# Kernel tuning notes

Measured on AMD Instinct MI355X. Metric: run time of the kernel, lower is better.

## Reference

```python
import jax, jax.numpy as jnp
import numpy as np

RANK = 16
ALPHA = 32.0
SCALING = ALPHA / RANK  # 2.0


def setup_inputs() -> dict:
    key = jax.random.key(0)
    k1, k2, k3, k4, k5 = jax.random.split(key, 5)
    B, S, D_IN, D_OUT = 4, 4096, 4096, 4096
    x = jax.random.normal(k1, (B, S, D_IN), dtype=jnp.float32)
    W = jax.random.normal(k2, (D_OUT, D_IN), dtype=jnp.float32) * 0.02
    b = jax.random.normal(k3, (D_OUT,), dtype=jnp.float32) * 0.02
    lora_A = jax.random.normal(k4, (RANK, D_IN), dtype=jnp.float32) * 0.02
    lora_B = jax.random.normal(k5, (D_OUT, RANK), dtype=jnp.float32) * 0.02
    return {"x": x, "W": W, "b": b, "lora_A": lora_A, "lora_B": lora_B}


def reference(x, W, b, lora_A, lora_B):
    # Base linear: y = x @ W^T + b
    base = jnp.einsum("bsd,od->bso", x, W) + b
    # LoRA delta: mathematically x @ (B @ A)^T * scaling == ((x @ A^T) @ B^T) * scaling.
    # We chain the two small rank-limited GEMMs (same math, efficient form).
    xa = jnp.einsum("bsd,rd->bsr", x, lora_A)           # [B,S,rank]
    lora_out = jnp.einsum("bsr,or->bso", xa, lora_B)    # [B,S,out]
    return base + SCALING * lora_out
```

## Files before the change

kernel.cpp:

```cpp
#include <hip/hip_runtime.h>
#include <hip/hip_bf16.h>
#include <cstdint>

constexpr int  KDIM  = 4096;
constexpr int  NDIM  = 4096;
constexpr long MDIM  = 16384;
constexpr int  RANK_ = 16;
constexpr float SCALE_ = 2.0f;

constexpr int BK = 64;
constexpr int NT = KDIM / BK;

using bf16x8 = __attribute__((ext_vector_type(8))) short;
using f32x4  = __attribute__((ext_vector_type(4))) float;

__device__ __forceinline__ void gload_lds16(const void* g, void* l) {
  __builtin_amdgcn_global_load_lds(
      (const __attribute__((address_space(1))) void*)g,
      (__attribute__((address_space(3))) void*)l, 16, 0, 0);
}

__device__ __forceinline__ unsigned short f2bf(float f) {
  union { float f; unsigned u; } v; v.f = f;
  unsigned r = v.u + 0x7FFFu + ((v.u >> 16) & 1u);
  return (unsigned short)(r >> 16);
}

#define LDF(P, OFF) (*reinterpret_cast<const bf16x8*>((P) + (OFF)))

__global__ __launch_bounds__(256) void fused_prep_kernel(
    const float* __restrict__ x,  const float* __restrict__ W,
    const float* __restrict__ lA, const float* __restrict__ lB,
    unsigned short* __restrict__ xb, unsigned short* __restrict__ Wp) {
  if (blockIdx.x < 512) {
    const long totW = (long)NDIM * KDIM / 8;
    for (long t = blockIdx.x * 256L + threadIdx.x; t < totW; t += 512L * 256) {
      const int o  = (int)(t / (KDIM / 8));
      const int d8 = (int)(t % (KDIM / 8)) * 8;
      const float4* w4 = reinterpret_cast<const float4*>(W + (size_t)o * KDIM + d8);
      float4 w0 = w4[0], w1 = w4[1];
      float acc[8] = {w0.x, w0.y, w0.z, w0.w, w1.x, w1.y, w1.z, w1.w};
#pragma unroll
      for (int r = 0; r < RANK_; ++r) {
        const float br = SCALE_ * lB[o * RANK_ + r];
        const float4* a4 = reinterpret_cast<const float4*>(lA + (size_t)r * KDIM + d8);
        float4 a0 = a4[0], a1 = a4[1];
        acc[0] += br * a0.x; acc[1] += br * a0.y; acc[2] += br * a0.z; acc[3] += br * a0.w;
        acc[4] += br * a1.x; acc[5] += br * a1.y; acc[6] += br * a1.z; acc[7] += br * a1.w;
      }
      uint4 o4;
      o4.x = (unsigned)f2bf(acc[0]) | ((unsigned)f2bf(acc[1]) << 16);
      o4.y = (unsigned)f2bf(acc[2]) | ((unsigned)f2bf(acc[3]) << 16);
      o4.z = (unsigned)f2bf(acc[4]) | ((unsigned)f2bf(acc[5]) << 16);
      o4.w = (unsigned)f2bf(acc[6]) | ((unsigned)f2bf(acc[7]) << 16);
      *reinterpret_cast<uint4*>(Wp + t * 8) = o4;
    }
  } else {
    const long totX = MDIM * KDIM / 8;
    for (long t = (blockIdx.x - 512) * 256L + threadIdx.x; t < totX;
         t += 3584L * 256) {
      const float4* p = reinterpret_cast<const float4*>(x + t * 8);
      float4 a = p[0], b = p[1];
      uint4 o4;
      o4.x = (unsigned)f2bf(a.x) | ((unsigned)f2bf(a.y) << 16);
      o4.y = (unsigned)f2bf(a.z) | ((unsigned)f2bf(a.w) << 16);
      o4.z = (unsigned)f2bf(b.x) | ((unsigned)f2bf(b.y) << 16);
      o4.w = (unsigned)f2bf(b.z) | ((unsigned)f2bf(b.w) << 16);
      *reinterpret_cast<uint4*>(xb + t * 8) = o4;
    }
  }
}

__global__ __launch_bounds__(512, 2) void gemm256_kernel(
    const unsigned short* __restrict__ A,
    const unsigned short* __restrict__ Bm,
    const float* __restrict__ bias,
    float* __restrict__ C) {
  __shared__ __align__(16) unsigned char lds[131072];

  const int tid  = threadIdx.x;
  const int wave = tid >> 6, lane = tid & 63;
  const int wm = wave >> 2, wn = wave & 3;
  const int r16 = lane & 15, hi = lane >> 4;
  const int swz5 = ((r16 >> 3) & 1) << 5;
  const int lrB = (wn & 1) * 64;

  const int orig = blockIdx.x;
  const int bid  = (orig & 7) * 128 + (orig >> 3);
  const int bcol = (bid & 15) * 256;
  const int brow = (bid >> 4) * 256;

  const int st_row = wave * 16 + (lane >> 2);
  const int st_col = ((lane & 3) * 8) ^ (((lane >> 5) & 1) << 4);
  const unsigned short* Asrc = A  + (size_t)(brow + st_row) * KDIM + st_col;
  const unsigned short* Bsrc = Bm + (size_t)(bcol + st_row) * KDIM + st_col;

  auto stageHalf = [&](unsigned char* base, int s, int tau) {
    const unsigned short* g = (s >= 2 ? Asrc + (size_t)(s - 2) * 128 * KDIM
                                      : Bsrc + (size_t)s * 128 * KDIM) + tau * BK;
    unsigned char* d = base + (wave << 10) + s * 16384;
    gload_lds16(g,      d);
    gload_lds16(g + 32, d + 8192);
  };

  const int laneoff = r16 * 64 + ((hi * 16) ^ swz5);
  const unsigned char* pA0 = lds + (2 + wm) * 16384 + laneoff;
  const unsigned char* pB0 = lds + (wn >> 1) * 16384 + lrB * 64 + laneoff;
  const unsigned char* pA1 = pA0 + 65536;
  const unsigned char* pB1 = pB0 + 65536;

  f32x4 acc[8][4];
#pragma unroll
  for (int m = 0; m < 8; ++m)
#pragma unroll
    for (int n = 0; n < 4; ++n) acc[m][n] = (f32x4){0.f, 0.f, 0.f, 0.f};

  unsigned char* const buf0 = lds;
  unsigned char* const buf1 = lds + 65536;

  stageHalf(buf0, 0, 0); stageHalf(buf0, 1, 0);
  stageHalf(buf0, 2, 0); stageHalf(buf0, 3, 0);
  stageHalf(buf1, 0, 1); stageHalf(buf1, 1, 1);
  asm volatile("s_waitcnt vmcnt(4)" ::: "memory");
  __builtin_amdgcn_s_barrier();

  bf16x8 xlo[4][2], xhi[4][2], wlo[2][2], whi[2][2];
#pragma unroll
  for (int m = 0; m < 4; ++m) {
    xlo[m][0] = LDF(pA0, m * 1024);
    xlo[m][1] = LDF(pA0, m * 1024 + 8192);
  }

#define KTILE(CB, NB, PA, PB, PAN, t)                                          \
  {                                                                            \
         \
    _Pragma("unroll")                                                          \
    for (int n = 0; n < 2; ++n) {                                              \
      wlo[n][0] = LDF(PB, n * 1024);                                           \
      wlo[n][1] = LDF(PB, n * 1024 + 8192);                                    \
    }                                                                          \
    _Pragma("unroll")                                                          \
    for (int n = 0; n < 2; ++n) {                                              \
      whi[n][0] = LDF(PB, (n + 2) * 1024);                                     \
      whi[n][1] = LDF(PB, (n + 2) * 1024 + 8192);                              \
    }                                                                          \
    if ((t) + 1 < NT) { stageHalf((NB), 2, (t) + 1);                           \
                        stageHalf((NB), 3, (t) + 1); }                         \
    __builtin_amdgcn_s_setprio(1);                                             \
    _Pragma("unroll")                                                          \
    for (int kk = 0; kk < 2; ++kk)                                             \
      _Pragma("unroll")                                                        \
      for (int m = 0; m < 4; ++m)                                              \
        _Pragma("unroll")                                                      \
        for (int n = 0; n < 2; ++n)                                            \
          acc[m][n] = __builtin_amdgcn_mfma_f32_16x16x32_bf16(                 \
              wlo[n][kk], xlo[m][kk], acc[m][n], 0, 0, 0);                     \
    __builtin_amdgcn_s_setprio(0);                                             \
    __builtin_amdgcn_s_barrier();                                              \
                               \
    _Pragma("unroll")                                                          \
    for (int m = 0; m < 4; ++m) {                                              \
      xhi[m][0] = LDF(PA, (m + 4) * 1024);                                     \
      xhi[m][1] = LDF(PA, (m + 4) * 1024 + 8192);                              \
    }                                                                          \
    __builtin_amdgcn_s_setprio(1);                                             \
    _Pragma("unroll")                                                          \
    for (int kk = 0; kk < 2; ++kk)                                             \
      _Pragma("unroll")                                                        \
      for (int m = 0; m < 4; ++m)                                              \
        _Pragma("unroll")                                                      \
        for (int n = 0; n < 2; ++n)                                            \
          acc[m][n + 2] = __builtin_amdgcn_mfma_f32_16x16x32_bf16(             \
              whi[n][kk], xlo[m][kk], acc[m][n + 2], 0, 0, 0);                 \
    __builtin_amdgcn_s_setprio(0);                                             \
    __builtin_amdgcn_s_barrier();                                              \
            \
    if ((t) + 2 < NT) { stageHalf((CB), 0, (t) + 2);                           \
                        stageHalf((CB), 1, (t) + 2); }                         \
    __builtin_amdgcn_s_setprio(1);                                             \
    _Pragma("unroll")                                                          \
    for (int kk = 0; kk < 2; ++kk)                                             \
      _Pragma("unroll")                                                        \
      for (int m = 0; m < 4; ++m)                                              \
        _Pragma("unroll")                                                      \
        for (int n = 0; n < 2; ++n)                                            \
          acc[m + 4][n + 2] = __builtin_amdgcn_mfma_f32_16x16x32_bf16(         \
              whi[n][kk], xhi[m][kk], acc[m + 4][n + 2], 0, 0, 0);             \
    __builtin_amdgcn_s_setprio(0);                                             \
    __builtin_amdgcn_s_barrier();                                              \
                      \
    if ((t) < NT - 2)       asm volatile("s_waitcnt vmcnt(4)" ::: "memory");   \
    else if ((t) == NT - 2) asm volatile("s_waitcnt vmcnt(0)" ::: "memory");   \
    __builtin_amdgcn_s_barrier();                                              \
    if ((t) + 1 < NT) {                                                        \
      _Pragma("unroll")                                                        \
      for (int m = 0; m < 4; ++m) {                                            \
        xlo[m][0] = LDF(PAN, m * 1024);                                        \
        xlo[m][1] = LDF(PAN, m * 1024 + 8192);                                 \
      }                                                                        \
    }                                                                          \
    __builtin_amdgcn_s_setprio(1);                                             \
    _Pragma("unroll")                                                          \
    for (int kk = 0; kk < 2; ++kk)                                             \
      _Pragma("unroll")                                                        \
      for (int m = 0; m < 4; ++m)                                              \
        _Pragma("unroll")                                                      \
        for (int n = 0; n < 2; ++n)                                            \
          acc[m + 4][n] = __builtin_amdgcn_mfma_f32_16x16x32_bf16(             \
              wlo[n][kk], xhi[m][kk], acc[m + 4][n], 0, 0, 0);                 \
    __builtin_amdgcn_s_setprio(0);                                             \
  }

  for (int tt = 0; tt < NT; tt += 2) {
    KTILE(buf0, buf1, pA0, pB0, pA1, tt);
    KTILE(buf1, buf0, pA1, pB1, pA0, tt + 1);
  }
#undef KTILE

#pragma unroll
  for (int n = 0; n < 4; ++n) {
    const int colb = bcol + wn * 64 + n * 16 + hi * 4;
    const f32x4 bv = *reinterpret_cast<const f32x4*>(&bias[colb]);
#pragma unroll
    for (int m = 0; m < 8; ++m) {
      const size_t row = (size_t)brow + wm * 128 + m * 16 + r16;
      f32x4 v = acc[m][n] + bv;
      *reinterpret_cast<f32x4*>(&C[row * NDIM + colb]) = v;
    }
  }
}

extern "C" void kernel_launch(void* const* d_in, const int* in_sizes, int n_in,
                              void* d_out, int out_size, void* d_ws, size_t ws_size,
                              hipStream_t stream) {
  const float* x  = (const float*)d_in[0];
  const float* W  = (const float*)d_in[1];
  const float* b  = (const float*)d_in[2];
  const float* lA = (const float*)d_in[3];
  const float* lB = (const float*)d_in[4];
  float* out = (float*)d_out;

  unsigned short* xb = (unsigned short*)d_ws;
  unsigned short* Wp = (unsigned short*)((char*)d_ws + (size_t)MDIM * KDIM * 2);

  fused_prep_kernel<<<4096, 256, 0, stream>>>(x, W, lA, lB, xb, Wp);
  gemm256_kernel<<<1024, 512, 0, stream>>>(xb, Wp, b, out);
}
```

Before: 589.3 us.

## Shrink GEMM block tile to 128x256 with BK=32 for higher occupancy

Replaces the 256x256 block tile (BK=64, 128KB LDS) with a 128x256 tile at BK=32 using 48KB of double-buffered LDS. The launch grid doubles to 2048 blocks and launch bounds now allow four blocks per CU. The K-loop staging and barriers are restructured to fit the smaller tile. The aim is more resident waves and better latency hiding, at the cost of lower arithmetic intensity per block, more global/LDS traffic per flop, and twice as many barriers per K.

```diff
diff --git a/kernel.cpp b/kernel.cpp
--- a/kernel.cpp
+++ b/kernel.cpp
@@ -8,8 +8,9 @@
 constexpr int  RANK_ = 16;
 constexpr float SCALE_ = 2.0f;
 
-constexpr int BK = 64;
+constexpr int BK = 32;
 constexpr int NT = KDIM / BK;
+constexpr int BUFB = 24576;
 
 using bf16x8 = __attribute__((ext_vector_type(8))) short;
 using f32x4  = __attribute__((ext_vector_type(4))) float;
@@ -71,149 +72,107 @@
   }
 }
 
-__global__ __launch_bounds__(512, 2) void gemm256_kernel(
+__global__ __launch_bounds__(512, 4) void gemm128_kernel(
     const unsigned short* __restrict__ A,
     const unsigned short* __restrict__ Bm,
     const float* __restrict__ bias,
     float* __restrict__ C) {
-  __shared__ __align__(16) unsigned char lds[131072];
+  __shared__ __align__(16) unsigned char lds[2 * BUFB];
 
   const int tid  = threadIdx.x;
   const int wave = tid >> 6, lane = tid & 63;
   const int wm = wave >> 2, wn = wave & 3;
   const int r16 = lane & 15, hi = lane >> 4;
   const int swz5 = ((r16 >> 3) & 1) << 5;
-  const int lrB = (wn & 1) * 64;
 
   const int orig = blockIdx.x;
-  const int bid  = (orig & 7) * 128 + (orig >> 3);
+  const int bid  = (orig & 7) * 256 + (orig >> 3);
   const int bcol = (bid & 15) * 256;
-  const int brow = (bid >> 4) * 256;
-
-  const int st_row = wave * 16 + (lane >> 2);
+  const int brow = (bid >> 4) * 128;
+
   const int st_col = ((lane & 3) * 8) ^ (((lane >> 5) & 1) << 4);
-  const unsigned short* Asrc = A  + (size_t)(brow + st_row) * KDIM + st_col;
-  const unsigned short* Bsrc = Bm + (size_t)(bcol + st_row) * KDIM + st_col;
-
-  auto stageHalf = [&](unsigned char* base, int s, int tau) {
-    const unsigned short* g = (s >= 2 ? Asrc + (size_t)(s - 2) * 128 * KDIM
-                                      : Bsrc + (size_t)s * 128 * KDIM) + tau * BK;
-    unsigned char* d = base + (wave << 10) + s * 16384;
-    gload_lds16(g,      d);
-    gload_lds16(g + 32, d + 8192);
+  const unsigned short* AsrcS =
+      A  + (size_t)(brow + wave * 16 + (lane >> 2)) * KDIM + st_col;
+  const unsigned short* BsrcS =
+      Bm + (size_t)(bcol + wave * 32 + (lane >> 2)) * KDIM + st_col;
+
+  auto stageA = [&](unsigned char* base, int tau) {
+    gload_lds16(AsrcS + (size_t)tau * BK, base + 16384 + (wave << 10));
   };
+  auto stageB = [&](unsigned char* base, int tau) {
+    const unsigned short* g = BsrcS + (size_t)tau * BK;
+    unsigned char* d = base + (wave << 11);
+    gload_lds16(g,                      d);
+    gload_lds16(g + (size_t)16 * KDIM,  d + 1024);
+  };
 
   const int laneoff = r16 * 64 + ((hi * 16) ^ swz5);
-  const unsigned char* pA0 = lds + (2 + wm) * 16384 + laneoff;
-  const unsigned char* pB0 = lds + (wn >> 1) * 16384 + lrB * 64 + laneoff;
-  const unsigned char* pA1 = pA0 + 65536;
-  const unsigned char* pB1 = pB0 + 65536;
-
-  f32x4 acc[8][4];
-#pragma unroll
-  for (int m = 0; m < 8; ++m)
+  const unsigned char* pB0 = lds + wn * 4096 + laneoff;
+  const unsigned char* pA0 = lds + 16384 + wm * 4096 + laneoff;
+  const unsigned char* pB1 = pB0 + BUFB;
+  const unsigned char* pA1 = pA0 + BUFB;
+
+  f32x4 acc[4][4];
+#pragma unroll
+  for (int m = 0; m < 4; ++m)
 #pragma unroll
     for (int n = 0; n < 4; ++n) acc[m][n] = (f32x4){0.f, 0.f, 0.f, 0.f};
 
   unsigned char* const buf0 = lds;
-  unsigned char* const buf1 = lds + 65536;
-
-  stageHalf(buf0, 0, 0); stageHalf(buf0, 1, 0);
-  stageHalf(buf0, 2, 0); stageHalf(buf0, 3, 0);
-  stageHalf(buf1, 0, 1); stageHalf(buf1, 1, 1);
-  asm volatile("s_waitcnt vmcnt(4)" ::: "memory");
+  unsigned char* const buf1 = lds + BUFB;
+
+  stageA(buf0, 0); stageB(buf0, 0);
+  stageA(buf1, 1); stageB(buf1, 1);
+  asm volatile("s_waitcnt vmcnt(3)" ::: "memory");
   __builtin_amdgcn_s_barrier();
 
-  bf16x8 xlo[4][2], xhi[4][2], wlo[2][2], whi[2][2];
-#pragma unroll
-  for (int m = 0; m < 4; ++m) {
-    xlo[m][0] = LDF(pA0, m * 1024);
-    xlo[m][1] = LDF(pA0, m * 1024 + 8192);
-  }
-
-#define KTILE(CB, NB, PA, PB, PAN, t)                                          \
+  bf16x8 x[4], w[4];
+#pragma unroll
+  for (int m = 0; m < 4; ++m) x[m] = LDF(pA0, m * 1024);
+  w[0] = LDF(pB0, 0);
+  w[1] = LDF(pB0, 1024);
+
+#define KTILE(PA, PB, PAN, PBN, CB, t)                                         \
   {                                                                            \
-         \
-    _Pragma("unroll")                                                          \
-    for (int n = 0; n < 2; ++n) {                                              \
-      wlo[n][0] = LDF(PB, n * 1024);                                           \
-      wlo[n][1] = LDF(PB, n * 1024 + 8192);                                    \
-    }                                                                          \
-    _Pragma("unroll")                                                          \
-    for (int n = 0; n < 2; ++n) {                                              \
-      whi[n][0] = LDF(PB, (n + 2) * 1024);                                     \
-      whi[n][1] = LDF(PB, (n + 2) * 1024 + 8192);                              \
-    }                                                                          \
-    if ((t) + 1 < NT) { stageHalf((NB), 2, (t) + 1);                           \
-                        stageHalf((NB), 3, (t) + 1); }                         \
+              \
+    w[2] = LDF(PB, 2 * 1024);                                                  \
+    w[3] = LDF(PB, 3 * 1024);                                                  \
+    if ((t) + 2 < NT) stageA((CB), (t) + 2);                                   \
     __builtin_amdgcn_s_setprio(1);                                             \
     _Pragma("unroll")                                                          \
-    for (int kk = 0; kk < 2; ++kk)                                             \
+    for (int m = 0; m < 4; ++m)                                                \
       _Pragma("unroll")                                                        \
-      for (int m = 0; m < 4; ++m)                                              \
-        _Pragma("unroll")                                                      \
-        for (int n = 0; n < 2; ++n)                                            \
-          acc[m][n] = __builtin_amdgcn_mfma_f32_16x16x32_bf16(                 \
-              wlo[n][kk], xlo[m][kk], acc[m][n], 0, 0, 0);                     \
+      for (int n = 0; n < 2; ++n)                                              \
+        acc[m][n] = __builtin_amdgcn_mfma_f32_16x16x32_bf16(                   \
+            w[n], x[m], acc[m][n], 0, 0, 0);                                   \
     __builtin_amdgcn_s_setprio(0);                                             \
+    if ((t) < NT - 2)       asm volatile("s_waitcnt vmcnt(1)" ::: "memory");   \
+    else if ((t) == NT - 2) asm volatile("s_waitcnt vmcnt(0)" ::: "memory");   \
     __builtin_amdgcn_s_barrier();                                              \
-                               \
-    _Pragma("unroll")                                                          \
-    for (int m = 0; m < 4; ++m) {                                              \
-      xhi[m][0] = LDF(PA, (m + 4) * 1024);                                     \
-      xhi[m][1] = LDF(PA, (m + 4) * 1024 + 8192);                              \
+         \
+    if ((t) + 1 < NT) {                                                        \
+      w[0] = LDF(PBN, 0);                                                      \
+      w[1] = LDF(PBN, 1024);                                                   \
     }                                                                          \
+    if ((t) + 2 < NT) stageB((CB), (t) + 2);                                   \
     __builtin_amdgcn_s_setprio(1);                                             \
     _Pragma("unroll")                                                          \
-    for (int kk = 0; kk < 2; ++kk)                                             \
+    for (int m = 0; m < 4; ++m)                                                \
       _Pragma("unroll")                                                        \
-      for (int m = 0; m < 4; ++m)                                              \
-        _Pragma("unroll")                                                      \
-        for (int n = 0; n < 2; ++n)                                            \
-          acc[m][n + 2] = __builtin_amdgcn_mfma_f32_16x16x32_bf16(             \
-              whi[n][kk], xlo[m][kk], acc[m][n + 2], 0, 0, 0);                 \
+      for (int n = 0; n < 2; ++n)                                              \
+        acc[m][n + 2] = __builtin_amdgcn_mfma_f32_16x16x32_bf16(               \
+            w[n + 2], x[m], acc[m][n + 2], 0, 0, 0);                           \
     __builtin_amdgcn_s_setprio(0);                                             \
-    __builtin_amdgcn_s_barrier();                                              \
-            \
-    if ((t) + 2 < NT) { stageHalf((CB), 0, (t) + 2);                           \
-                        stageHalf((CB), 1, (t) + 2); }                         \
-    __builtin_amdgcn_s_setprio(1);                                             \
-    _Pragma("unroll")                                                          \
-    for (int kk = 0; kk < 2; ++kk)                                             \
-      _Pragma("unroll")                                                        \
-      for (int m = 0; m < 4; ++m)                                              \
-        _Pragma("unroll")                                                      \
-        for (int n = 0; n < 2; ++n)                                            \
-          acc[m + 4][n + 2] = __builtin_amdgcn_mfma_f32_16x16x32_bf16(         \
-              whi[n][kk], xhi[m][kk], acc[m + 4][n + 2], 0, 0, 0);             \
-    __builtin_amdgcn_s_setprio(0);                                             \
-    __builtin_amdgcn_s_barrier();                                              \
-                      \
-    if ((t) < NT - 2)       asm volatile("s_waitcnt vmcnt(4)" ::: "memory");   \
-    else if ((t) == NT - 2) asm volatile("s_waitcnt vmcnt(0)" ::: "memory");   \
-    __builtin_amdgcn_s_barrier();                                              \
     if ((t) + 1 < NT) {                                                        \
       _Pragma("unroll")                                                        \
-      for (int m = 0; m < 4; ++m) {                                            \
-        xlo[m][0] = LDF(PAN, m * 1024);                                        \
-        xlo[m][1] = LDF(PAN, m * 1024 + 8192);                                 \
-      }                                                                        \
+      for (int m = 0; m < 4; ++m) x[m] = LDF(PAN, m * 1024);                   \
     }                                                                          \
-    __builtin_amdgcn_s_setprio(1);                                             \
-    _Pragma("unroll")                                                          \
-    for (int kk = 0; kk < 2; ++kk)                                             \
-      _Pragma("unroll")                                                        \
-      for (int m = 0; m < 4; ++m)                                              \
-        _Pragma("unroll")                                                      \
-        for (int n = 0; n < 2; ++n)                                            \
-          acc[m + 4][n] = __builtin_amdgcn_mfma_f32_16x16x32_bf16(             \
-              wlo[n][kk], xhi[m][kk], acc[m + 4][n], 0, 0, 0);                 \
-    __builtin_amdgcn_s_setprio(0);                                             \
+    __builtin_amdgcn_s_barrier();                                              \
   }
 
   for (int tt = 0; tt < NT; tt += 2) {
-    KTILE(buf0, buf1, pA0, pB0, pA1, tt);
-    KTILE(buf1, buf0, pA1, pB1, pA0, tt + 1);
+    KTILE(pA0, pB0, pA1, pB1, buf0, tt);
+    KTILE(pA1, pB1, pA0, pB0, buf1, tt + 1);
   }
 #undef KTILE
 
@@ -222,8 +181,8 @@
     const int colb = bcol + wn * 64 + n * 16 + hi * 4;
     const f32x4 bv = *reinterpret_cast<const f32x4*>(&bias[colb]);
 #pragma unroll
-    for (int m = 0; m < 8; ++m) {
-      const size_t row = (size_t)brow + wm * 128 + m * 16 + r16;
+    for (int m = 0; m < 4; ++m) {
+      const size_t row = (size_t)brow + wm * 64 + m * 16 + r16;
       f32x4 v = acc[m][n] + bv;
       *reinterpret_cast<f32x4*>(&C[row * NDIM + colb]) = v;
     }
@@ -244,5 +203,5 @@
   unsigned short* Wp = (unsigned short*)((char*)d_ws + (size_t)MDIM * KDIM * 2);
 
   fused_prep_kernel<<<4096, 256, 0, stream>>>(x, W, lA, lB, xb, Wp);
-  gemm256_kernel<<<1024, 512, 0, stream>>>(xb, Wp, b, out);
-}
+  gemm128_kernel<<<2048, 512, 0, stream>>>(xb, Wp, b, out);
+}
```

Result: slower. 685.2 us (+16.3%).
